# Kernel tuning notes

Measured on AMD Instinct MI355X. Metric: run time of the kernel, lower is better.

## Reference

```python
import math
import jax, jax.numpy as jnp
import numpy as np

N_HEAD = 8


def setup_inputs() -> dict:
    key = jax.random.key(0)
    ks = jax.random.split(key, 9)
    B, S, D = 4, 2048, 512
    s = 1.0 / math.sqrt(D)
    return {
        "x": jax.random.normal(ks[0], (B, S, D), jnp.float32),
        "Wq": jax.random.normal(ks[1], (D, D), jnp.float32) * s,
        "bq": jax.random.normal(ks[2], (D,), jnp.float32) * s,
        "Wk": jax.random.normal(ks[3], (D, D), jnp.float32) * s,
        "bk": jax.random.normal(ks[4], (D,), jnp.float32) * s,
        "Wv": jax.random.normal(ks[5], (D, D), jnp.float32) * s,
        "bv": jax.random.normal(ks[6], (D,), jnp.float32) * s,
        "Wo": jax.random.normal(ks[7], (D, D), jnp.float32) * s,
        "bo": jax.random.normal(ks[8], (D,), jnp.float32) * s,
    }


def reference(x, Wq, bq, Wk, bk, Wv, bv, Wo, bo):
    B, S, D = x.shape
    H = N_HEAD
    hd = D // H
    # projections -> [B, H, S, hd]
    def split_heads(y):
        return y.reshape(B, S, H, hd).transpose(0, 2, 1, 3)
    q = split_heads(x @ Wq + bq)
    k = split_heads(x @ Wk + bk)
    v = split_heads(x @ Wv + bv)
    scale = 1.0 / math.sqrt(hd)
    scores = jnp.einsum("bhqd,bhkd->bhqk", q, k) * scale  # [B,H,S,S]
    attn = jax.nn.softmax(scores, axis=-1)
    ctx = jnp.einsum("bhqk,bhkd->bhqd", attn, v)  # [B,H,S,hd]
    ctx = ctx.transpose(0, 2, 1, 3).reshape(B, S, D)
    out = ctx @ Wo + bo
    avg_attn = attn.mean(axis=1)  # [B,S,S]
    return out, avg_attn
```

## Files before the change

kernel.cpp:

```cpp
#include <hip/hip_runtime.h>

typedef __bf16 bf16;
typedef __bf16 bf16x8 __attribute__((ext_vector_type(8)));
typedef float  f32x4  __attribute__((ext_vector_type(4)));
typedef float  f32x16 __attribute__((ext_vector_type(16)));
typedef unsigned u32x4 __attribute__((ext_vector_type(4)));

#define MFMA16(a,b,c) __builtin_amdgcn_mfma_f32_16x16x32_bf16((a),(b),(c),0,0,0)
#define MFMA32(a,b,c) __builtin_amdgcn_mfma_f32_32x32x16_bf16((a),(b),(c),0,0,0)

#define BATCH 4
#define SEQ   2048
#define DIM   512
#define NH    8
#define HD    64
#define QSCALE 0.18033688f

__device__ __forceinline__ bf16x8 ldsfrag(const bf16* t, int row, int kc, int quad){
    int unit = ((kc << 2) + quad) ^ (row & 7);
    return *(const bf16x8*)(t + row * 64 + unit * 8);
}
__device__ __forceinline__ bf16x8 ldsfrag32(const bf16* t, int row, int unit){
    return *(const bf16x8*)(t + row * 64 + ((unit ^ (row & 7)) << 3));
}

__device__ __forceinline__ void stage64x64(const bf16* src, long rowStride, bf16* dst, int tid){
#pragma unroll
    for (int rnd = 0; rnd < 2; ++rnd){
        int sid = tid + rnd * 256;
        int row = sid >> 3, s = sid & 7;
        bf16x8 val = *(const bf16x8*)(src + (long)row * rowStride + s * 8);
        *(bf16x8*)(dst + row * 64 + ((s ^ (row & 7)) << 3)) = val;
    }
}

__device__ __forceinline__ unsigned packbf(float lo, float hi){
    unsigned short lb = __builtin_bit_cast(unsigned short, (bf16)lo);
    unsigned short hb = __builtin_bit_cast(unsigned short, (bf16)hi);
    return (unsigned)lb | ((unsigned)hb << 16);
}

__global__ __launch_bounds__(256) void cvt_x(const float* __restrict__ x, bf16* __restrict__ xb){
    int i = blockIdx.x * 256 + threadIdx.x;
    float4 f = ((const float4*)x)[i];
    bf16* o = xb + 4 * (long)i;
    o[0] = (bf16)f.x; o[1] = (bf16)f.y; o[2] = (bf16)f.z; o[3] = (bf16)f.w;
}

__global__ __launch_bounds__(256) void cvt_wt(const float* __restrict__ Wq, const float* __restrict__ Wk,
                                              const float* __restrict__ Wv, const float* __restrict__ Wo,
                                              bf16* __restrict__ WTb){
    int z = blockIdx.z;
    const float* W = (z == 0) ? Wq : (z == 1) ? Wk : (z == 2) ? Wv : Wo;
    bf16* WT = WTb + (long)z * DIM * DIM;
    __shared__ float lt[32 * 33];
    int t = threadIdx.x, r0 = t >> 5, c = t & 31;
    int k0 = blockIdx.x * 32, n0 = blockIdx.y * 32;
#pragma unroll
    for (int i = 0; i < 4; ++i){
        int row = r0 + i * 8;
        lt[row * 33 + c] = W[(long)(k0 + row) * DIM + n0 + c];
    }
    __syncthreads();
#pragma unroll
    for (int i = 0; i < 4; ++i){
        int nr = r0 + i * 8;
        WT[(long)(n0 + nr) * DIM + k0 + c] = (bf16)lt[c * 33 + nr];
    }
}

__global__ __launch_bounds__(256) void gemm_qkv(const bf16* __restrict__ X, const bf16* __restrict__ WTb,
                                                const float* __restrict__ bq, const float* __restrict__ bk,
                                                const float* __restrict__ bv, bf16* __restrict__ outb){
    __shared__ __align__(16) bf16 lA[128 * 64];
    __shared__ __align__(16) bf16 lB[128 * 64];
    int z = blockIdx.z;
    const bf16* WT = WTb + (long)z * DIM * DIM;
    const float* bias = (z == 0) ? bq : (z == 1) ? bk : bv;
    float qs = (z == 0) ? QSCALE : 1.0f;
    bf16* out = outb + (long)z * BATCH * SEQ * DIM;
    int tid = threadIdx.x, lane = tid & 63, w = tid >> 6;
    int wm = w >> 1, wn = w & 1;
    int m0 = blockIdx.y * 128, n0 = blockIdx.x * 128;
    int r16 = lane & 15, quad = lane >> 4;
    f32x4 zz = {0.f, 0.f, 0.f, 0.f};
    f32x4 acc[4][4];
#pragma unroll
    for (int a = 0; a < 4; ++a)
#pragma unroll
        for (int b2 = 0; b2 < 4; ++b2) acc[a][b2] = zz;

    for (int k0 = 0; k0 < DIM; k0 += 64){
        __syncthreads();
#pragma unroll
        for (int rnd = 0; rnd < 4; ++rnd){
            int sid = tid + rnd * 256;
            int row = sid >> 3, s = sid & 7;
            *(bf16x8*)(lA + row * 64 + ((s ^ (row & 7)) << 3)) =
                *(const bf16x8*)(X + (long)(m0 + row) * DIM + k0 + s * 8);
            *(bf16x8*)(lB + row * 64 + ((s ^ (row & 7)) << 3)) =
                *(const bf16x8*)(WT + (long)(n0 + row) * DIM + k0 + s * 8);
        }
        __syncthreads();
#pragma unroll
        for (int kc = 0; kc < 2; ++kc){
            bf16x8 aF[4], bF[4];
#pragma unroll
            for (int i = 0; i < 4; ++i){
                aF[i] = ldsfrag(lA, wm * 64 + i * 16 + r16, kc, quad);
                bF[i] = ldsfrag(lB, wn * 64 + i * 16 + r16, kc, quad);
            }
#pragma unroll
            for (int rb = 0; rb < 4; ++rb)
#pragma unroll
                for (int nb = 0; nb < 4; ++nb)
                    acc[rb][nb] = MFMA16(aF[rb], bF[nb], acc[rb][nb]);
        }
    }
#pragma unroll
    for (int nb = 0; nb < 4; ++nb){
        int col = n0 + wn * 64 + nb * 16 + r16;
        float bv_ = bias[col];
        int hh = col >> 6, d = col & 63;
#pragma unroll
        for (int rb = 0; rb < 4; ++rb)
#pragma unroll
            for (int r = 0; r < 4; ++r){
                int row = m0 + wm * 64 + rb * 16 + quad * 4 + r;
                int bb = row >> 11, s = row & 2047;
                out[((long)(bb * NH + hh) * SEQ + s) * HD + d] = (bf16)((acc[rb][nb][r] + bv_) * qs);
            }
    }
}

__global__ __launch_bounds__(256) void vtrans(const bf16* __restrict__ v, bf16* __restrict__ vT){
    __shared__ bf16 lt[64 * 72];
    int tid = threadIdx.x;
    int s0 = blockIdx.x * 64;
    int bh = blockIdx.z * NH + blockIdx.y;
#pragma unroll
    for (int rnd = 0; rnd < 2; ++rnd){
        int sid = tid + rnd * 256;
        int row = sid >> 3, sg = sid & 7;
        *(bf16x8*)(lt + row * 72 + sg * 8) =
            *(const bf16x8*)(v + ((long)bh * SEQ + s0 + row) * HD + sg * 8);
    }
    __syncthreads();
#pragma unroll
    for (int rnd = 0; rnd < 2; ++rnd){
        int sid = tid + rnd * 256;
        int d = sid >> 3, sg = sid & 7;
        bf16x8 o;
#pragma unroll
        for (int j = 0; j < 8; ++j) o[j] = lt[(sg * 8 + j) * 72 + d];
        *(bf16x8*)(vT + ((long)bh * HD + d) * SEQ + s0 + sg * 8) = o;
    }
}

__global__ __launch_bounds__(512) void attn_flash(const bf16* __restrict__ q, const bf16* __restrict__ k,
                                                  const bf16* __restrict__ vT, bf16* __restrict__ ctx,
                                                  float* __restrict__ llv_g){
    __shared__ __align__(16) bf16 lQ[128 * 64];
    __shared__ __align__(16) bf16 lKV[2][2][8192];
    int tid = threadIdx.x, lane = tid & 63, w = tid >> 6;
    int g = w >> 2, wq = w & 3;
    int t256 = tid & 255;
    int lin = blockIdx.x + (blockIdx.y << 4) + (blockIdx.z << 7);
    int task = ((lin & 7) << 6) + (lin >> 3);
    int qt = task & 15, h = (task >> 4) & 7, b = task >> 7;
    int bh = b * NH + h;
    int q0 = qt * 128;
    int row32 = lane & 31, half = lane >> 5;

    int r0_ = t256 >> 3, s_ = t256 & 7;
    const bf16* kbase = k + ((long)bh * SEQ + g * (SEQ / 2)) * HD;
    const bf16* vbase = vT + (long)bh * HD * SEQ + g * (SEQ / 2);
    bf16x8 kr0, kr1, vr0, vr1;

    auto LOADREGS = [&](int jt){
        int j0 = jt * 64;
        kr0 = *(const bf16x8*)(kbase + (long)(j0 + r0_) * HD + s_ * 8);
        kr1 = *(const bf16x8*)(kbase + (long)(j0 + r0_ + 32) * HD + s_ * 8);
        vr0 = *(const bf16x8*)(vbase + (long)r0_ * SEQ + j0 + s_ * 8);
        vr1 = *(const bf16x8*)(vbase + (long)(r0_ + 32) * SEQ + j0 + s_ * 8);
    };
    auto WRITELDS = [&](int buf){
        bf16* lK = lKV[g][buf];
        bf16* lV = lK + 4096;
        int u = (s_ ^ (r0_ & 7)) << 3;
        *(bf16x8*)(lK + r0_ * 64 + u) = kr0;
        *(bf16x8*)(lK + (r0_ + 32) * 64 + u) = kr1;
        *(bf16x8*)(lV + r0_ * 64 + u) = vr0;
        *(bf16x8*)(lV + (r0_ + 32) * 64 + u) = vr1;
    };

    LOADREGS(0);
    {
        const bf16* src = q + ((long)bh * SEQ + q0) * HD;
#pragma unroll
        for (int rnd = 0; rnd < 2; ++rnd){
            int sid = tid + rnd * 512;
            int row = sid >> 3, s = sid & 7;
            *(bf16x8*)(lQ + row * 64 + ((s ^ (row & 7)) << 3)) =
                *(const bf16x8*)(src + (long)row * HD + s * 8);
        }
    }
    __syncthreads();
    bf16x8 qF[4];
#pragma unroll
    for (int s = 0; s < 4; ++s) qF[s] = ldsfrag32(lQ, wq * 32 + row32, 2 * s + half);

    f32x16 ctxacc[2], lsacc;
#pragma unroll
    for (int i = 0; i < 16; ++i){ ctxacc[0][i] = 0.f; ctxacc[1][i] = 0.f; lsacc[i] = 0.f; }
    bf16x8 onesv;
#pragma unroll
    for (int i = 0; i < 8; ++i) onesv[i] = (bf16)1.0f;

    auto COMPUTE = [&](int buf){
        const bf16* lK = lKV[g][buf];
        const bf16* lV = lK + 4096;
        __builtin_amdgcn_s_setprio(1);
#pragma unroll
        for (int kb = 0; kb < 2; ++kb){
            f32x16 sacc;
#pragma unroll
            for (int i = 0; i < 16; ++i) sacc[i] = 0.f;
#pragma unroll
            for (int s = 0; s < 4; ++s)
                sacc = MFMA32(ldsfrag32(lK, kb * 32 + row32, 2 * s + half), qF[s], sacc);
            float p[16];
#pragma unroll
            for (int reg = 0; reg < 16; ++reg)
                p[reg] = __builtin_amdgcn_exp2f(sacc[reg]);
            unsigned Wp[4][2];
#pragma unroll
            for (int b2 = 0; b2 < 4; ++b2)
#pragma unroll
                for (int j = 0; j < 2; ++j)
                    Wp[b2][j] = packbf(p[4 * b2 + 2 * j], p[4 * b2 + 2 * j + 1]);
#pragma unroll
            for (int K = 0; K < 2; ++K){
                unsigned X0 = Wp[2 * K + 1][0], X1 = Wp[2 * K + 1][1];
                unsigned Y0 = Wp[2 * K][0],     Y1 = Wp[2 * K][1];
                unsigned X0p = (unsigned)__shfl_xor((int)X0, 32, 64);
                unsigned X1p = (unsigned)__shfl_xor((int)X1, 32, 64);
                unsigned Y0p = (unsigned)__shfl_xor((int)Y0, 32, 64);
                unsigned Y1p = (unsigned)__shfl_xor((int)Y1, 32, 64);
                u32x4 wv;
                wv[0] = half ? X0p : Y0;
                wv[1] = half ? X1p : Y1;
                wv[2] = half ? X0  : Y0p;
                wv[3] = half ? X1  : Y1p;
                bf16x8 pa = __builtin_bit_cast(bf16x8, wv);
                int ks = 2 * kb + K;
                lsacc = MFMA32(pa, onesv, lsacc);
#pragma unroll
                for (int db = 0; db < 2; ++db)
                    ctxacc[db] = MFMA32(pa, ldsfrag32(lV, db * 32 + row32, 2 * ks + half), ctxacc[db]);
            }
        }
        __builtin_amdgcn_s_setprio(0);
    };

    WRITELDS(0);
    __syncthreads();
#pragma unroll 1
    for (int t = 0; t < 15; ++t){
        LOADREGS(t + 1);
        COMPUTE(t & 1);
        WRITELDS((t + 1) & 1);
        __syncthreads();
    }
    COMPUTE(1);

    __syncthreads();
    float* xch = (float*)&lKV[0][0][0];
    if (g == 1){
        float* dst = xch + ((wq << 6) + lane) * 49;
#pragma unroll
        for (int i = 0; i < 16; ++i){
            dst[i] = ctxacc[0][i]; dst[16 + i] = ctxacc[1][i]; dst[32 + i] = lsacc[i];
        }
    }
    __syncthreads();
    if (g == 0){
        const float* src2 = xch + ((wq << 6) + lane) * 49;
#pragma unroll
        for (int i = 0; i < 16; ++i){
            ctxacc[0][i] += src2[i]; ctxacc[1][i] += src2[16 + i]; lsacc[i] += src2[32 + i];
        }
        float rinv[16];
#pragma unroll
        for (int reg = 0; reg < 16; ++reg) rinv[reg] = 1.0f / lsacc[reg];
#pragma unroll
        for (int db = 0; db < 2; ++db)
#pragma unroll
            for (int reg = 0; reg < 16; ++reg){
                int qr = (reg & 3) + 8 * (reg >> 2) + 4 * half;
                long srow = q0 + wq * 32 + qr;
                ctx[((long)b * SEQ + srow) * DIM + h * HD + db * 32 + row32] =
                    (bf16)(ctxacc[db][reg] * rinv[reg]);
            }
        if (row32 == 0)
#pragma unroll
            for (int reg = 0; reg < 16; ++reg){
                int qr = (reg & 3) + 8 * (reg >> 2) + 4 * half;
                llv_g[(long)bh * SEQ + q0 + wq * 32 + qr] = -__log2f(lsacc[reg]) - 3.0f;
            }
    }
}

__global__ __launch_bounds__(256) void attn_avg(const bf16* __restrict__ q, const bf16* __restrict__ k,
                                                const float* __restrict__ llv_g, float* __restrict__ avg){
    __shared__ __align__(16) bf16 lQ[64 * 64];
    __shared__ __align__(16) bf16 lK[64 * 64];
    __shared__ __align__(16) float lsOut[4][16 * 65];
    int lin  = blockIdx.x + (blockIdx.y << 5) + (blockIdx.z << 10);
    int task = ((lin & 7) << 9) + (lin >> 3);
    int qt = task & 31;
    int jt = (task >> 5) & 31;
    int b  = task >> 10;
    int tid = threadIdx.x, lane = tid & 63, w = tid >> 6;
    int r16 = lane & 15, quad = lane >> 4;
    int qbase = qt * 64;
    int j0 = jt * 64;

    int r0_ = tid >> 3, s_ = tid & 7;
    int u_ = (s_ ^ (r0_ & 7)) << 3;
    bf16x8 qr0, qr1, kr0, kr1;
    auto LOADA = [&](int hh){
        long hA = (long)b * NH + hh;
        const bf16* qh = q + (hA * SEQ + qbase) * HD;
        const bf16* kh = k + (hA * SEQ + j0) * HD;
        qr0 = *(const bf16x8*)(qh + (long)r0_ * HD + s_ * 8);
        qr1 = *(const bf16x8*)(qh + (long)(r0_ + 32) * HD + s_ * 8);
        kr0 = *(const bf16x8*)(kh + (long)r0_ * HD + s_ * 8);
        kr1 = *(const bf16x8*)(kh + (long)(r0_ + 32) * HD + s_ * 8);
    };
    auto WRITEA = [&](){
        *(bf16x8*)(lQ + r0_ * 64 + u_) = qr0;
        *(bf16x8*)(lQ + (r0_ + 32) * 64 + u_) = qr1;
        *(bf16x8*)(lK + r0_ * 64 + u_) = kr0;
        *(bf16x8*)(lK + (r0_ + 32) * 64 + u_) = kr1;
    };

    f32x4 psum[4];
#pragma unroll
    for (int cb = 0; cb < 4; ++cb) psum[cb] = (f32x4){0.f, 0.f, 0.f, 0.f};

    LOADA(0);
    WRITEA();
    __syncthreads();
#pragma unroll 1
    for (int hh = 0; hh < NH; ++hh){
        if (hh < NH - 1) LOADA(hh + 1);
        f32x4 llv = *(const f32x4*)(llv_g + ((long)b * NH + hh) * SEQ + qbase + w * 16 + quad * 4);
        bf16x8 aF0 = ldsfrag(lQ, w * 16 + r16, 0, quad);
        bf16x8 aF1 = ldsfrag(lQ, w * 16 + r16, 1, quad);
#pragma unroll
        for (int cb = 0; cb < 4; ++cb){
            f32x4 sa = MFMA16(aF0, ldsfrag(lK, cb * 16 + r16, 0, quad), llv);
            sa = MFMA16(aF1, ldsfrag(lK, cb * 16 + r16, 1, quad), sa);
#pragma unroll
            for (int r = 0; r < 4; ++r)
                psum[cb][r] += __builtin_amdgcn_exp2f(sa[r]);
        }
        __syncthreads();
        if (hh < NH - 1){
            WRITEA();
            __syncthreads();
        }
    }

#pragma unroll
    for (int cb = 0; cb < 4; ++cb)
#pragma unroll
        for (int r = 0; r < 4; ++r)
            lsOut[w][(quad * 4 + r) * 65 + cb * 16 + r16] = psum[cb][r];
#pragma unroll
    for (int i = 0; i < 4; ++i){
        int row  = ((i >> 1) << 3) + (lane >> 3);
        int col4 = ((i & 1) << 5) + ((lane & 7) << 2);
        f32x4 v = *(const f32x4*)(&lsOut[w][row * 65 + col4]);
        __builtin_nontemporal_store(v,
            (f32x4*)&avg[((long)b * SEQ + qbase + w * 16 + row) * SEQ + j0 + col4]);
    }
}

__global__ __launch_bounds__(256) void gemm_out(const bf16* __restrict__ CTX, const bf16* __restrict__ WT,
                                                const float* __restrict__ bo, float* __restrict__ out){
    __shared__ __align__(16) bf16 lA[128 * 64];
    __shared__ __align__(16) bf16 lB[128 * 64];
    int tid = threadIdx.x, lane = tid & 63, w = tid >> 6;
    int wm = w >> 1, wn = w & 1;
    int m0 = blockIdx.y * 128, n0 = blockIdx.x * 128;
    int r16 = lane & 15, quad = lane >> 4;
    f32x4 zz = {0.f, 0.f, 0.f, 0.f};
    f32x4 acc[4][4];
#pragma unroll
    for (int a = 0; a < 4; ++a)
#pragma unroll
        for (int b2 = 0; b2 < 4; ++b2) acc[a][b2] = zz;

    for (int k0 = 0; k0 < DIM; k0 += 64){
        __syncthreads();
#pragma unroll
        for (int rnd = 0; rnd < 4; ++rnd){
            int sid = tid + rnd * 256;
            int row = sid >> 3, s = sid & 7;
            *(bf16x8*)(lA + row * 64 + ((s ^ (row & 7)) << 3)) =
                *(const bf16x8*)(CTX + (long)(m0 + row) * DIM + k0 + s * 8);
            *(bf16x8*)(lB + row * 64 + ((s ^ (row & 7)) << 3)) =
                *(const bf16x8*)(WT + (long)(n0 + row) * DIM + k0 + s * 8);
        }
        __syncthreads();
#pragma unroll
        for (int kc = 0; kc < 2; ++kc){
            bf16x8 aF[4], bF[4];
#pragma unroll
            for (int i = 0; i < 4; ++i){
                aF[i] = ldsfrag(lA, wm * 64 + i * 16 + r16, kc, quad);
                bF[i] = ldsfrag(lB, wn * 64 + i * 16 + r16, kc, quad);
            }
#pragma unroll
            for (int rb2 = 0; rb2 < 4; ++rb2)
#pragma unroll
                for (int nb = 0; nb < 4; ++nb)
                    acc[rb2][nb] = MFMA16(aF[rb2], bF[nb], acc[rb2][nb]);
        }
    }
#pragma unroll
    for (int nb = 0; nb < 4; ++nb){
        int col = n0 + wn * 64 + nb * 16 + r16;
        float bv_ = bo[col];
#pragma unroll
        for (int rb2 = 0; rb2 < 4; ++rb2)
#pragma unroll
            for (int r = 0; r < 4; ++r){
                int row = m0 + wm * 64 + rb2 * 16 + quad * 4 + r;
                out[(long)row * DIM + col] = acc[rb2][nb][r] + bv_;
            }
    }
}

extern "C" void kernel_launch(void* const* d_in, const int* in_sizes, int n_in,
                              void* d_out, int out_size, void* d_ws, size_t ws_size,
                              hipStream_t stream) {
    const float* x  = (const float*)d_in[0];
    const float* Wq = (const float*)d_in[1];
    const float* bq = (const float*)d_in[2];
    const float* Wk = (const float*)d_in[3];
    const float* bk = (const float*)d_in[4];
    const float* Wv = (const float*)d_in[5];
    const float* bv = (const float*)d_in[6];
    const float* Wo = (const float*)d_in[7];
    const float* bo = (const float*)d_in[8];
    float* out = (float*)d_out;

    char* ws = (char*)d_ws;
    bf16*  xb   = (bf16*)(ws);
    bf16*  WT   = (bf16*)(ws + 8388608);
    bf16*  qb   = (bf16*)(ws + 10485760);
    bf16*  kb   = qb + (long)BATCH * SEQ * DIM;
    bf16*  vb   = kb + (long)BATCH * SEQ * DIM;
    bf16*  vT   = (bf16*)(ws + 35651584);
    bf16*  ctx  = (bf16*)(ws + 44040192);
    float* llv  = (float*)(ws + 52428800);

    cvt_x    <<<4096, 256, 0, stream>>>(x, xb);
    cvt_wt   <<<dim3(16, 16, 4), 256, 0, stream>>>(Wq, Wk, Wv, Wo, WT);
    gemm_qkv <<<dim3(4, 64, 3), 256, 0, stream>>>(xb, WT, bq, bk, bv, qb);
    vtrans   <<<dim3(32, 8, 4), 256, 0, stream>>>(vb, vT);
    attn_flash<<<dim3(16, 8, 4), 512, 0, stream>>>(qb, kb, vT, ctx, llv);
    attn_avg <<<dim3(32, 32, 4), 256, 0, stream>>>(qb, kb, llv, out + (long)BATCH * SEQ * DIM);
    gemm_out <<<dim3(4, 64), 256, 0, stream>>>(ctx, WT + 3L * DIM * DIM, bo, out);
}
```

Measured before the change: 238.4 us.

## Merge conversion kernels and tail kernels, use direct global-to-LDS loads in QKV GEMM

Merges the x and weight conversion kernels into one launch, and merges the attention-average kernel with the output projection GEMM into one launch that dispatches on block index and shares an LDS pool. The QKV GEMM now stages tiles with global_load_lds, applying the XOR swizzle to the source address instead of the LDS destination. This is meant to cut launch gaps and tail underutilisation, and to avoid the register round trip during staging. In exchange, the merged kernel needs a larger LDS pool, which may lower occupancy for the attention-average blocks.

Result: slower. 257.5 us (+8.0%).

```diff
diff --git a/kernel.cpp b/kernel.cpp
--- a/kernel.cpp
+++ b/kernel.cpp
@@ -8,6 +8,10 @@
 
 #define MFMA16(a,b,c) __builtin_amdgcn_mfma_f32_16x16x32_bf16((a),(b),(c),0,0,0)
 #define MFMA32(a,b,c) __builtin_amdgcn_mfma_f32_32x32x16_bf16((a),(b),(c),0,0,0)
+
+#define GLOAD16(g, l) __builtin_amdgcn_global_load_lds( \
+    (const __attribute__((address_space(1))) void*)(g), \
+    (__attribute__((address_space(3))) void*)(l), 16, 0, 0)
 
 #define BATCH 4
 #define SEQ   2048
@@ -24,48 +28,41 @@
     return *(const bf16x8*)(t + row * 64 + ((unit ^ (row & 7)) << 3));
 }
 
-__device__ __forceinline__ void stage64x64(const bf16* src, long rowStride, bf16* dst, int tid){
-#pragma unroll
-    for (int rnd = 0; rnd < 2; ++rnd){
-        int sid = tid + rnd * 256;
-        int row = sid >> 3, s = sid & 7;
-        bf16x8 val = *(const bf16x8*)(src + (long)row * rowStride + s * 8);
-        *(bf16x8*)(dst + row * 64 + ((s ^ (row & 7)) << 3)) = val;
-    }
-}
-
 __device__ __forceinline__ unsigned packbf(float lo, float hi){
     unsigned short lb = __builtin_bit_cast(unsigned short, (bf16)lo);
     unsigned short hb = __builtin_bit_cast(unsigned short, (bf16)hi);
     return (unsigned)lb | ((unsigned)hb << 16);
 }
 
-__global__ __launch_bounds__(256) void cvt_x(const float* __restrict__ x, bf16* __restrict__ xb){
-    int i = blockIdx.x * 256 + threadIdx.x;
-    float4 f = ((const float4*)x)[i];
-    bf16* o = xb + 4 * (long)i;
-    o[0] = (bf16)f.x; o[1] = (bf16)f.y; o[2] = (bf16)f.z; o[3] = (bf16)f.w;
-}
-
-__global__ __launch_bounds__(256) void cvt_wt(const float* __restrict__ Wq, const float* __restrict__ Wk,
-                                              const float* __restrict__ Wv, const float* __restrict__ Wo,
-                                              bf16* __restrict__ WTb){
-    int z = blockIdx.z;
+__global__ __launch_bounds__(256) void cvt_fused(const float* __restrict__ x, bf16* __restrict__ xb,
+                                                 const float* __restrict__ Wq, const float* __restrict__ Wk,
+                                                 const float* __restrict__ Wv, const float* __restrict__ Wo,
+                                                 bf16* __restrict__ WTb){
+    __shared__ float lt[32 * 33];
+    int bid = blockIdx.x;
+    if (bid < 4096){
+        int i = bid * 256 + threadIdx.x;
+        float4 f = ((const float4*)x)[i];
+        bf16* o = xb + 4 * (long)i;
+        o[0] = (bf16)f.x; o[1] = (bf16)f.y; o[2] = (bf16)f.z; o[3] = (bf16)f.w;
+        return;
+    }
+    int c = bid - 4096;
+    int z = c >> 8, rem = c & 255;
     const float* W = (z == 0) ? Wq : (z == 1) ? Wk : (z == 2) ? Wv : Wo;
     bf16* WT = WTb + (long)z * DIM * DIM;
-    __shared__ float lt[32 * 33];
-    int t = threadIdx.x, r0 = t >> 5, c = t & 31;
-    int k0 = blockIdx.x * 32, n0 = blockIdx.y * 32;
+    int t = threadIdx.x, r0 = t >> 5, cc = t & 31;
+    int k0 = (rem & 15) * 32, n0 = (rem >> 4) * 32;
 #pragma unroll
     for (int i = 0; i < 4; ++i){
         int row = r0 + i * 8;
-        lt[row * 33 + c] = W[(long)(k0 + row) * DIM + n0 + c];
+        lt[row * 33 + cc] = W[(long)(k0 + row) * DIM + n0 + cc];
     }
     __syncthreads();
 #pragma unroll
     for (int i = 0; i < 4; ++i){
         int nr = r0 + i * 8;
-        WT[(long)(n0 + nr) * DIM + k0 + c] = (bf16)lt[c * 33 + nr];
+        WT[(long)(n0 + nr) * DIM + k0 + cc] = (bf16)lt[cc * 33 + nr];
     }
 }
 
@@ -93,13 +90,13 @@
     for (int k0 = 0; k0 < DIM; k0 += 64){
         __syncthreads();
 #pragma unroll
-        for (int rnd = 0; rnd < 4; ++rnd){
-            int sid = tid + rnd * 256;
-            int row = sid >> 3, s = sid & 7;
-            *(bf16x8*)(lA + row * 64 + ((s ^ (row & 7)) << 3)) =
-                *(const bf16x8*)(X + (long)(m0 + row) * DIM + k0 + s * 8);
-            *(bf16x8*)(lB + row * 64 + ((s ^ (row & 7)) << 3)) =
-                *(const bf16x8*)(WT + (long)(n0 + row) * DIM + k0 + s * 8);
+        for (int c = 0; c < 4; ++c){
+            int sid = c * 256 + tid;
+            int row = sid >> 3, u = sid & 7;
+            int s = u ^ (row & 7);
+            int base = (c * 256 + (tid & ~63)) * 8;
+            GLOAD16(X  + (long)(m0 + row) * DIM + k0 + s * 8, lA + base);
+            GLOAD16(WT + (long)(n0 + row) * DIM + k0 + s * 8, lB + base);
         }
         __syncthreads();
 #pragma unroll
@@ -311,18 +308,77 @@
     }
 }
 
-__global__ __launch_bounds__(256) void attn_avg(const bf16* __restrict__ q, const bf16* __restrict__ k,
-                                                const float* __restrict__ llv_g, float* __restrict__ avg){
-    __shared__ __align__(16) bf16 lQ[64 * 64];
-    __shared__ __align__(16) bf16 lK[64 * 64];
-    __shared__ __align__(16) float lsOut[4][16 * 65];
-    int lin  = blockIdx.x + (blockIdx.y << 5) + (blockIdx.z << 10);
+__global__ __launch_bounds__(256) void tail_fused(const bf16* __restrict__ q, const bf16* __restrict__ k,
+                                                  const float* __restrict__ llv_g, float* __restrict__ avg,
+                                                  const bf16* __restrict__ CTX, const bf16* __restrict__ WT,
+                                                  const float* __restrict__ bo, float* __restrict__ out){
+    __shared__ __align__(16) char pool[33280];
+    int bid = blockIdx.x;
+    int tid = threadIdx.x, lane = tid & 63, w = tid >> 6;
+    int r16 = lane & 15, quad = lane >> 4;
+    f32x4 zz = {0.f, 0.f, 0.f, 0.f};
+
+    if (bid < 256){
+        bf16* lA = (bf16*)pool;
+        bf16* lB = (bf16*)(pool + 16384);
+        int wm = w >> 1, wn = w & 1;
+        int m0 = (bid >> 2) * 128, n0 = (bid & 3) * 128;
+        f32x4 acc[4][4];
+#pragma unroll
+        for (int a = 0; a < 4; ++a)
+#pragma unroll
+            for (int b2 = 0; b2 < 4; ++b2) acc[a][b2] = zz;
+
+        for (int k0 = 0; k0 < DIM; k0 += 64){
+            __syncthreads();
+#pragma unroll
+            for (int rnd = 0; rnd < 4; ++rnd){
+                int sid = tid + rnd * 256;
+                int row = sid >> 3, s = sid & 7;
+                *(bf16x8*)(lA + row * 64 + ((s ^ (row & 7)) << 3)) =
+                    *(const bf16x8*)(CTX + (long)(m0 + row) * DIM + k0 + s * 8);
+                *(bf16x8*)(lB + row * 64 + ((s ^ (row & 7)) << 3)) =
+                    *(const bf16x8*)(WT + (long)(n0 + row) * DIM + k0 + s * 8);
+            }
+            __syncthreads();
+#pragma unroll
+            for (int kc = 0; kc < 2; ++kc){
+                bf16x8 aF[4], bF[4];
+#pragma unroll
+                for (int i = 0; i < 4; ++i){
+                    aF[i] = ldsfrag(lA, wm * 64 + i * 16 + r16, kc, quad);
+                    bF[i] = ldsfrag(lB, wn * 64 + i * 16 + r16, kc, quad);
+                }
+#pragma unroll
+                for (int rb2 = 0; rb2 < 4; ++rb2)
+#pragma unroll
+                    for (int nb = 0; nb < 4; ++nb)
+                        acc[rb2][nb] = MFMA16(aF[rb2], bF[nb], acc[rb2][nb]);
+            }
+        }
+#pragma unroll
+        for (int nb = 0; nb < 4; ++nb){
+            int col = n0 + wn * 64 + nb * 16 + r16;
+            float bv_ = bo[col];
+#pragma unroll
+            for (int rb2 = 0; rb2 < 4; ++rb2)
+#pragma unroll
+                for (int r = 0; r < 4; ++r){
+                    int row = m0 + wm * 64 + rb2 * 16 + quad * 4 + r;
+                    out[(long)row * DIM + col] = acc[rb2][nb][r] + bv_;
+                }
+        }
+        return;
+    }
+
+    bf16*  lQ = (bf16*)pool;
+    bf16*  lK = (bf16*)(pool + 8192);
+    float* lsO = (float*)(pool + 16384) + w * (16 * 65);
+    int lin  = bid - 256;
     int task = ((lin & 7) << 9) + (lin >> 3);
     int qt = task & 31;
     int jt = (task >> 5) & 31;
     int b  = task >> 10;
-    int tid = threadIdx.x, lane = tid & 63, w = tid >> 6;
-    int r16 = lane & 15, quad = lane >> 4;
     int qbase = qt * 64;
     int j0 = jt * 64;
 
@@ -347,7 +403,7 @@
 
     f32x4 psum[4];
 #pragma unroll
-    for (int cb = 0; cb < 4; ++cb) psum[cb] = (f32x4){0.f, 0.f, 0.f, 0.f};
+    for (int cb = 0; cb < 4; ++cb) psum[cb] = zz;
 
     LOADA(0);
     WRITEA();
@@ -377,70 +433,14 @@
     for (int cb = 0; cb < 4; ++cb)
 #pragma unroll
         for (int r = 0; r < 4; ++r)
-            lsOut[w][(quad * 4 + r) * 65 + cb * 16 + r16] = psum[cb][r];
+            lsO[(quad * 4 + r) * 65 + cb * 16 + r16] = psum[cb][r];
 #pragma unroll
     for (int i = 0; i < 4; ++i){
         int row  = ((i >> 1) << 3) + (lane >> 3);
         int col4 = ((i & 1) << 5) + ((lane & 7) << 2);
-        f32x4 v = *(const f32x4*)(&lsOut[w][row * 65 + col4]);
+        f32x4 v = *(const f32x4*)(&lsO[row * 65 + col4]);
         __builtin_nontemporal_store(v,
             (f32x4*)&avg[((long)b * SEQ + qbase + w * 16 + row) * SEQ + j0 + col4]);
-    }
-}
-
-__global__ __launch_bounds__(256) void gemm_out(const bf16* __restrict__ CTX, const bf16* __restrict__ WT,
-                                                const float* __restrict__ bo, float* __restrict__ out){
-    __shared__ __align__(16) bf16 lA[128 * 64];
-    __shared__ __align__(16) bf16 lB[128 * 64];
-    int tid = threadIdx.x, lane = tid & 63, w = tid >> 6;
-    int wm = w >> 1, wn = w & 1;
-    int m0 = blockIdx.y * 128, n0 = blockIdx.x * 128;
-    int r16 = lane & 15, quad = lane >> 4;
-    f32x4 zz = {0.f, 0.f, 0.f, 0.f};
-    f32x4 acc[4][4];
-#pragma unroll
-    for (int a = 0; a < 4; ++a)
-#pragma unroll
-        for (int b2 = 0; b2 < 4; ++b2) acc[a][b2] = zz;
-
-    for (int k0 = 0; k0 < DIM; k0 += 64){
-        __syncthreads();
-#pragma unroll
-        for (int rnd = 0; rnd < 4; ++rnd){
-            int sid = tid + rnd * 256;
-            int row = sid >> 3, s = sid & 7;
-            *(bf16x8*)(lA + row * 64 + ((s ^ (row & 7)) << 3)) =
-                *(const bf16x8*)(CTX + (long)(m0 + row) * DIM + k0 + s * 8);
-            *(bf16x8*)(lB + row * 64 + ((s ^ (row & 7)) << 3)) =
-                *(const bf16x8*)(WT + (long)(n0 + row) * DIM + k0 + s * 8);
-        }
-        __syncthreads();
-#pragma unroll
-        for (int kc = 0; kc < 2; ++kc){
-            bf16x8 aF[4], bF[4];
-#pragma unroll
-            for (int i = 0; i < 4; ++i){
-                aF[i] = ldsfrag(lA, wm * 64 + i * 16 + r16, kc, quad);
-                bF[i] = ldsfrag(lB, wn * 64 + i * 16 + r16, kc, quad);
-            }
-#pragma unroll
-            for (int rb2 = 0; rb2 < 4; ++rb2)
-#pragma unroll
-                for (int nb = 0; nb < 4; ++nb)
-                    acc[rb2][nb] = MFMA16(aF[rb2], bF[nb], acc[rb2][nb]);
-        }
-    }
-#pragma unroll
-    for (int nb = 0; nb < 4; ++nb){
-        int col = n0 + wn * 64 + nb * 16 + r16;
-        float bv_ = bo[col];
-#pragma unroll
-        for (int rb2 = 0; rb2 < 4; ++rb2)
-#pragma unroll
-            for (int r = 0; r < 4; ++r){
-                int row = m0 + wm * 64 + rb2 * 16 + quad * 4 + r;
-                out[(long)row * DIM + col] = acc[rb2][nb][r] + bv_;
-            }
     }
 }
 
@@ -468,11 +468,10 @@
     bf16*  ctx  = (bf16*)(ws + 44040192);
     float* llv  = (float*)(ws + 52428800);
 
-    cvt_x    <<<4096, 256, 0, stream>>>(x, xb);
-    cvt_wt   <<<dim3(16, 16, 4), 256, 0, stream>>>(Wq, Wk, Wv, Wo, WT);
-    gemm_qkv <<<dim3(4, 64, 3), 256, 0, stream>>>(xb, WT, bq, bk, bv, qb);
-    vtrans   <<<dim3(32, 8, 4), 256, 0, stream>>>(vb, vT);
+    cvt_fused <<<5120, 256, 0, stream>>>(x, xb, Wq, Wk, Wv, Wo, WT);
+    gemm_qkv  <<<dim3(4, 64, 3), 256, 0, stream>>>(xb, WT, bq, bk, bv, qb);
+    vtrans    <<<dim3(32, 8, 4), 256, 0, stream>>>(vb, vT);
     attn_flash<<<dim3(16, 8, 4), 512, 0, stream>>>(qb, kb, vT, ctx, llv);
-    attn_avg <<<dim3(32, 32, 4), 256, 0, stream>>>(qb, kb, llv, out + (long)BATCH * SEQ * DIM);
-    gemm_out <<<dim3(4, 64), 256, 0, stream>>>(ctx, WT + 3L * DIM * DIM, bo, out);
-}
+    tail_fused<<<4352, 256, 0, stream>>>(qb, kb, llv, out + (long)BATCH * SEQ * DIM,
+                                         ctx, WT + 3L * DIM * DIM, bo, out);
+}
```
